# Optimization experiments

Hardware: AMD Instinct MI355X
Metric: run time of the kernel (lower is better)

Reference implementation:

```python
import jax, jax.numpy as jnp
import numpy as np

N_NODES = 100000
N_EDGES = 1600000
NUM_GRAPHS = 128
IN_DIM, HID, NCLS = 128, 64, 10


def setup_inputs() -> dict:
    key = jax.random.key(0)
    ks = jax.random.split(key, 12)
    inp = {
        'x': jax.random.normal(ks[0], (N_NODES, IN_DIM), jnp.float32),
        'edge_index': jax.random.randint(ks[1], (2, N_EDGES), 0, N_NODES),
        'edge_weight': jax.random.uniform(ks[2], (N_EDGES,), jnp.float32),
        'batch': jnp.sort(jax.random.randint(ks[3], (N_NODES,), 0, NUM_GRAPHS)),
        'W1': jax.random.normal(ks[4], (IN_DIM, HID), jnp.float32) * 0.05,
        'b1': jnp.zeros((HID,), jnp.float32),
        'W2': jax.random.normal(ks[5], (HID, HID), jnp.float32) * 0.05,
        'b2': jnp.zeros((HID,), jnp.float32),
        'Wc1': jax.random.normal(ks[6], (HID, HID // 2), jnp.float32) * 0.05,
        'bc1': jnp.zeros((HID // 2,), jnp.float32),
        'Wc2': jax.random.normal(ks[7], (HID // 2, NCLS), jnp.float32) * 0.05,
        'bc2': jnp.zeros((NCLS,), jnp.float32),
    }
    return inp


def _gcn_conv(x, row, col, ew, W, b, n):
    # PyG GCNConv: add self-loops (weight 1), symmetric normalization,
    # transform then aggregate: out[col] += norm * (xW)[row]
    loop = jnp.arange(n)
    r = jnp.concatenate([row, loop])
    c = jnp.concatenate([col, loop])
    w = jnp.concatenate([ew, jnp.ones((n,), ew.dtype)])
    deg = jax.ops.segment_sum(w, c, num_segments=n)
    dinv = jnp.where(deg > 0, jax.lax.rsqrt(deg), 0.0)
    norm = dinv[r] * w * dinv[c]          # [E+N]
    h = x @ W                              # [N, out]
    msg = h[r] * norm[:, None]             # [E+N, out]
    out = jax.ops.segment_sum(msg, c, num_segments=n)
    return out + b


def reference(x, edge_index, edge_weight, batch, W1, b1, W2, b2, Wc1, bc1, Wc2, bc2):
    n = x.shape[0]
    row, col = edge_index[0], edge_index[1]
    h = jax.nn.relu(_gcn_conv(x, row, col, edge_weight, W1, b1, n))
    # dropout p=0.5 is identity in eval mode
    h = jax.nn.relu(_gcn_conv(h, row, col, edge_weight, W2, b2, n))
    # global mean pool over batch indices
    sums = jax.ops.segment_sum(h, batch, num_segments=NUM_GRAPHS)
    cnts = jax.ops.segment_sum(jnp.ones((n,), h.dtype), batch, num_segments=NUM_GRAPHS)
    pooled = sums / jnp.clip(cnts, 1.0)[:, None]   # [G, HID]
    z = jax.nn.relu(pooled @ Wc1 + bc1)
    return z @ Wc2 + bc2                            # [G, NCLS]
```

## Files before the change

kernel.cpp:

```cpp
#include <hip/hip_runtime.h>
#include <hip/hip_fp16.h>


#define TPB 256
#define FIX_SCALE 16777216.0f
#define BKT_BITS 8
#define PART_BLOCKS 256

typedef _Float16 f16x8 __attribute__((ext_vector_type(8)));
typedef float f32x4 __attribute__((ext_vector_type(4)));

__device__ __forceinline__ int lower_bound_i(const int* __restrict__ a, int n, int key) {
    int lo = 0, hi = n;
    while (lo < hi) {
        int mid = (lo + hi) >> 1;
        if (a[mid] < key) lo = mid + 1; else hi = mid;
    }
    return lo;
}

__global__ __launch_bounds__(256) void k_histA(const int* __restrict__ col, int E, int CH,
                                               int K, int* __restrict__ bh) {
    __shared__ int hist[512];
    int b = blockIdx.x, t = threadIdx.x;
    for (int i = t; i < K; i += 256) hist[i] = 0;
    __syncthreads();
    int s = b * CH, e = min(E, s + CH);
    for (int i = s + t; i < e; i += 256) atomicAdd(&hist[col[i] >> BKT_BITS], 1);
    __syncthreads();
    for (int i = t; i < K; i += 256) bh[i * PART_BLOCKS + b] = hist[i];
}

__global__ void k_scan_partial(const int* __restrict__ cnt, int* __restrict__ bsums, int n) {
    __shared__ int red[4];
    int b = blockIdx.x, t = threadIdx.x;
    int base = b * 1024;
    int s = 0;
#pragma unroll
    for (int i = 0; i < 4; i++) {
        int idx = base + t + i * TPB;
        if (idx < n) s += cnt[idx];
    }
#pragma unroll
    for (int off = 32; off > 0; off >>= 1) s += __shfl_down(s, off);
    if ((t & 63) == 0) red[t >> 6] = s;
    __syncthreads();
    if (t == 0) bsums[b] = red[0] + red[1] + red[2] + red[3];
}

__global__ void k_scan_bsums(int* __restrict__ bsums, int nb) {
    int l = threadIdx.x;
    int carry = 0;
    for (int base = 0; base < nb; base += 64) {
        int i = base + l;
        int v = (i < nb) ? bsums[i] : 0;
        int orig = v;
#pragma unroll
        for (int off = 1; off < 64; off <<= 1) {
            int x = __shfl_up(v, off);
            if (l >= off) v += x;
        }
        if (i < nb) bsums[i] = v - orig + carry;
        carry += __shfl(v, 63);
    }
}

__global__ void k_scan_final(const int* __restrict__ cnt, const int* __restrict__ boffs,
                             int* __restrict__ offs, int n) {
    __shared__ int ts[TPB];
    int b = blockIdx.x, t = threadIdx.x;
    int base = b * 1024 + 4 * t;
    int v[4]; int s = 0;
#pragma unroll
    for (int i = 0; i < 4; i++) {
        int idx = base + i;
        v[i] = (idx < n) ? cnt[idx] : 0;
        s += v[i];
    }
    ts[t] = s; __syncthreads();
    for (int off = 1; off < 256; off <<= 1) {
        int x = (t >= off) ? ts[t - off] : 0;
        __syncthreads();
        ts[t] += x;
        __syncthreads();
    }
    int run = ts[t] - s + boffs[b];
#pragma unroll
    for (int i = 0; i < 4; i++) {
        int idx = base + i;
        if (idx < n) offs[idx] = run;
        run += v[i];
    }
}

__global__ __launch_bounds__(256) void k_partB(const int* __restrict__ row,
                                               const int* __restrict__ col,
                                               const float* __restrict__ ew,
                                               const int* __restrict__ bhs,
                                               int E, int CH, int K,
                                               int2* __restrict__ part2) {
    __shared__ int cur[512];
    int b = blockIdx.x, t = threadIdx.x;
    for (int i = t; i < K; i += 256) cur[i] = bhs[i * PART_BLOCKS + b];
    __syncthreads();
    int s = b * CH, e = min(E, s + CH);
    for (int i = s + t; i < e; i += 256) {
        int c = col[i];
        int pos = atomicAdd(&cur[c >> BKT_BITS], 1);
        part2[pos] = make_int2(row[i] | ((c & 255) << 20), __float_as_int(ew[i]));
    }
}

__global__ __launch_bounds__(256) void k_csrC(const int2* __restrict__ part2,
                                              const int* __restrict__ bhs,
                                              int K, int N, int E,
                                              int* __restrict__ offs, int* __restrict__ cnt,
                                              float* __restrict__ dinv,
                                              int2* __restrict__ csr) {
    __shared__ int lcnt[256];
    __shared__ unsigned lew[256];
    __shared__ int lcur[256];
    __shared__ int ts[256];
    int k = blockIdx.x, t = threadIdx.x;
    int n0 = k << BKT_BITS;
    lcnt[t] = 0; lew[t] = 0;
    __syncthreads();
    int estart = bhs[k * PART_BLOCKS];
    int eend   = (k + 1 < K) ? bhs[(k + 1) * PART_BLOCKS] : E;
    for (int i = estart + t; i < eend; i += 256) {
        int2 v = part2[i];
        int c = (v.x >> 20) & 255;
        atomicAdd(&lcnt[c], 1);
        float w = __int_as_float(v.y);
        atomicAdd(&lew[c], (unsigned)(w * FIX_SCALE + 0.5f));
    }
    __syncthreads();
    int myc = lcnt[t];
    ts[t] = myc; __syncthreads();
    for (int off = 1; off < 256; off <<= 1) {
        int x = (t >= off) ? ts[t - off] : 0;
        __syncthreads();
        ts[t] += x;
        __syncthreads();
    }
    int goff = estart + ts[t] - myc;
    int node = n0 + t;
    if (node < N) {
        offs[node] = goff;
        cnt[node]  = myc;
        float deg = 1.0f + (float)((double)lew[t] * (1.0 / 16777216.0));
        dinv[node] = 1.0f / sqrtf(deg);
    }
    lcur[t] = goff;
    __syncthreads();
    for (int i = estart + t; i < eend; i += 256) {
        int2 v = part2[i];
        int c = (v.x >> 20) & 255;
        int pos = atomicAdd(&lcur[c], 1);
        csr[pos] = make_int2(v.x & 0xFFFFF, v.y);
    }
}

__global__ void k_prepW(const float* __restrict__ W1, const float* __restrict__ W2,
                        __half* __restrict__ Wt1, __half* __restrict__ Wt2) {
    int t = threadIdx.x;
    for (int i = t; i < 64 * 128; i += 256) {
        int c = i >> 7, k = i & 127;
        Wt1[i] = (__half)W1[k * 64 + c];
    }
    for (int i = t; i < 64 * 64; i += 256) {
        int c = i >> 6, k = i & 63;
        Wt2[i] = (__half)W2[k * 64 + c];
    }
}

template <int K>
__global__ __launch_bounds__(256) void k_matmul_mfma(const float* __restrict__ X,
                                                     const __half* __restrict__ Wt,
                                                     const float* __restrict__ dinv,
                                                     __half* __restrict__ Hh, int n) {
    const int l = threadIdx.x & 63;
    const int w = threadIdx.x >> 6;
    const int rowBase = blockIdx.x * 64 + w * 16;
    const int r = l & 15;
    const int q = l >> 4;
    const int arow = rowBase + r;
    const bool rv = arow < n;

    f32x4 acc[4] = {{0.f, 0.f, 0.f, 0.f}, {0.f, 0.f, 0.f, 0.f},
                    {0.f, 0.f, 0.f, 0.f}, {0.f, 0.f, 0.f, 0.f}};

#pragma unroll
    for (int k0 = 0; k0 < K; k0 += 32) {
        f16x8 a = {};
        if (rv) {
            const float4 x0 = *reinterpret_cast<const float4*>(&X[(size_t)arow * K + k0 + 8 * q]);
            const float4 x1 = *reinterpret_cast<const float4*>(&X[(size_t)arow * K + k0 + 8 * q + 4]);
            a[0] = (_Float16)x0.x; a[1] = (_Float16)x0.y;
            a[2] = (_Float16)x0.z; a[3] = (_Float16)x0.w;
            a[4] = (_Float16)x1.x; a[5] = (_Float16)x1.y;
            a[6] = (_Float16)x1.z; a[7] = (_Float16)x1.w;
        }
#pragma unroll
        for (int ct = 0; ct < 4; ct++) {
            const f16x8 b = *reinterpret_cast<const f16x8*>(
                &Wt[(size_t)(ct * 16 + r) * K + k0 + 8 * q]);
            acc[ct] = __builtin_amdgcn_mfma_f32_16x16x32_f16(a, b, acc[ct], 0, 0, 0);
        }
    }

#pragma unroll
    for (int i = 0; i < 4; i++) {
        int r2 = rowBase + 4 * q + i;
        if (r2 < n) {
            float dv = dinv[r2];
#pragma unroll
            for (int ct = 0; ct < 4; ct++)
                Hh[(size_t)r2 * 64 + ct * 16 + r] = (__half)(acc[ct][i] * dv);
        }
    }
}

__global__ __launch_bounds__(256) void k_aggregate(
    const __half2* __restrict__ hp2, const int* __restrict__ offs,
    const int* __restrict__ cnt, const int2* __restrict__ csr,
    const float* __restrict__ dinv, const float* __restrict__ bias,
    float* __restrict__ out, int n) {
    const int lane = threadIdx.x & 63;
    const int epar = lane >> 5;
    const int lpos = lane & 31;
    const int node = blockIdx.x * 4 + (threadIdx.x >> 6);
    if (node >= n) return;
    const int c = cnt[node];
    const int s = offs[node];

    int2 mc = make_int2(node, 0);
    if (lane < c) mc = csr[s + lane];
    const int cc = min(c, 64);
    const int npairs = (cc + 1) >> 1;
    const int p8 = (npairs + 7) & ~7;

    float ax[8] = {0.f, 0.f, 0.f, 0.f, 0.f, 0.f, 0.f, 0.f};
    float ay[8] = {0.f, 0.f, 0.f, 0.f, 0.f, 0.f, 0.f, 0.f};

    for (int p = 0; p < p8; p += 8) {
#pragma unroll
        for (int i = 0; i < 8; i++) {
            int idx = 2 * (p + i) + epar;
            int src = __shfl(mc.x, idx);
            float w = __int_as_float(__shfl(mc.y, idx));
            float2 f = __half22float2(hp2[(size_t)src * 32 + lpos]);
            ax[i] = fmaf(f.x, w, ax[i]);
            ay[i] = fmaf(f.y, w, ay[i]);
        }
    }
    float tx = ((ax[0] + ax[1]) + (ax[2] + ax[3])) + ((ax[4] + ax[5]) + (ax[6] + ax[7]));
    float ty = ((ay[0] + ay[1]) + (ay[2] + ay[3])) + ((ay[4] + ay[5]) + (ay[6] + ay[7]));
    tx += __shfl(tx, lane ^ 32);
    ty += __shfl(ty, lane ^ 32);

    for (int j = 64; j < c; ++j) {
        int2 e = csr[s + j];
        float2 f = __half22float2(hp2[(size_t)e.x * 32 + lpos]);
        float w = __int_as_float(e.y);
        tx = fmaf(f.x, w, tx);
        ty = fmaf(f.y, w, ty);
    }

    if (epar == 0) {
        float2 sv = __half22float2(hp2[(size_t)node * 32 + lpos]);
        const float2 bv = *reinterpret_cast<const float2*>(&bias[lpos * 2]);
        float dv = dinv[node];
        float rx = fmaf(tx + sv.x, dv, bv.x);
        float ry = fmaf(ty + sv.y, dv, bv.y);
        float2 o = make_float2(fmaxf(rx, 0.f), fmaxf(ry, 0.f));
        *reinterpret_cast<float2*>(&out[(size_t)node * 64 + lpos * 2]) = o;
    }
}

__global__ __launch_bounds__(1024) void k_pool_head(
    const float* __restrict__ h, const int* __restrict__ batch, int n,
    const float* __restrict__ Wc1, const float* __restrict__ bc1,
    const float* __restrict__ Wc2, const float* __restrict__ bc2,
    float* __restrict__ out) {
    const int g = blockIdx.x;
    const int t = threadIdx.x;
    const int lane = t & 63, w = t >> 6;
    __shared__ float sums[16][64];
    __shared__ float pooled[64];
    __shared__ float z[32];

    int start = lower_bound_i(batch, n, g);
    int end   = lower_bound_i(batch, n, g + 1);

    float acc = 0.f;
    for (int i = start + w; i < end; i += 16)
        acc += h[(size_t)i * 64 + lane];
    sums[w][lane] = acc;
    __syncthreads();
    if (w == 0) {
        float v = 0.f;
#pragma unroll
        for (int k = 0; k < 16; k++) v += sums[k][lane];
        float c = (float)(end - start);
        pooled[lane] = v / fmaxf(c, 1.0f);
    }
    __syncthreads();
    if (t < 32) {
        float a = bc1[t];
        for (int k = 0; k < 64; k++) a = fmaf(pooled[k], Wc1[k * 32 + t], a);
        z[t] = fmaxf(a, 0.f);
    }
    __syncthreads();
    if (t < 10) {
        float a = bc2[t];
        for (int k = 0; k < 32; k++) a = fmaf(z[k], Wc2[k * 10 + t], a);
        out[g * 10 + t] = a;
    }
}

extern "C" void kernel_launch(void* const* d_in, const int* in_sizes, int n_in,
                              void* d_out, int out_size, void* d_ws, size_t ws_size,
                              hipStream_t stream) {
    const float* x    = (const float*)d_in[0];
    const int*   ei   = (const int*)d_in[1];
    const float* ew   = (const float*)d_in[2];
    const int*   bat  = (const int*)d_in[3];
    const float* W1   = (const float*)d_in[4];
    const float* b1   = (const float*)d_in[5];
    const float* W2   = (const float*)d_in[6];
    const float* b2   = (const float*)d_in[7];
    const float* Wc1  = (const float*)d_in[8];
    const float* bc1  = (const float*)d_in[9];
    const float* Wc2  = (const float*)d_in[10];
    const float* bc2  = (const float*)d_in[11];
    float* out = (float*)d_out;

    const int N = in_sizes[0] / 128;
    const int E = in_sizes[2];
    const int G = out_size / 10;
    const int K = (N + 255) >> BKT_BITS;
    const int KB = K * PART_BLOCKS;
    const int CH = (E + PART_BLOCKS - 1) / PART_BLOCKS;

    const int* row = ei;
    const int* col = ei + E;

    char* p = (char*)d_ws;
    auto alloc = [&](size_t bytes) -> void* {
        void* r = (void*)p;
        p += (bytes + 255) & ~(size_t)255;
        return r;
    };
    int*    bh    = (int*)   alloc((size_t)KB * 4);
    int*    bhs   = (int*)   alloc((size_t)KB * 4);
    int*    bsums = (int*)   alloc(8192);
    int*    offs  = (int*)   alloc((size_t)N * 4);
    int*    cnt   = (int*)   alloc((size_t)N * 4);
    float*  dinv  = (float*) alloc((size_t)N * 4);
    __half* Wt1   = (__half*)alloc(64 * 128 * 2);
    __half* Wt2   = (__half*)alloc(64 * 64 * 2);
    int2*   csr   = (int2*)  alloc((size_t)E * 8);
    size_t hbytes = (size_t)N * 64 * 2;
    size_t pbytes = (size_t)E * 8;
    char*   hbase = (char*)  alloc(hbytes > pbytes ? hbytes : pbytes);
    float*  o     = (float*) alloc((size_t)N * 64 * 4);
    int2*   part2 = (int2*)  hbase;
    __half* h     = (__half*)hbase;

    const int NB = (KB + 1023) / 1024;

    k_prepW<<<1, 256, 0, stream>>>(W1, W2, Wt1, Wt2);

    k_histA<<<PART_BLOCKS, 256, 0, stream>>>(col, E, CH, K, bh);
    k_scan_partial<<<NB, TPB, 0, stream>>>(bh, bsums, KB);
    k_scan_bsums<<<1, 64, 0, stream>>>(bsums, NB);
    k_scan_final<<<NB, TPB, 0, stream>>>(bh, bsums, bhs, KB);
    k_partB<<<PART_BLOCKS, 256, 0, stream>>>(row, col, ew, bhs, E, CH, K, part2);
    k_csrC<<<K, 256, 0, stream>>>(part2, bhs, K, N, E, offs, cnt, dinv, csr);

    const int gb_mm = (N + 63) / 64;
    const int gb_ag = (N + 3) / 4;

    k_matmul_mfma<128><<<gb_mm, 256, 0, stream>>>(x, Wt1, dinv, h, N);
    k_aggregate<<<gb_ag, 256, 0, stream>>>((const __half2*)h, offs, cnt, csr, dinv, b1, o, N);
    k_matmul_mfma<64><<<gb_mm, 256, 0, stream>>>(o, Wt2, dinv, h, N);
    k_aggregate<<<gb_ag, 256, 0, stream>>>((const __half2*)h, offs, cnt, csr, dinv, b2, o, N);
    k_pool_head<<<G, 1024, 0, stream>>>(o, bat, N, Wc1, bc1, Wc2, bc2, out);
}
```

Baseline: 198.7 us.

## Store aggregate outputs in fp16, split pooling across blocks, fold weight prep

The aggregate kernels now write their hidden activations as fp16 instead of fp32. The second matmul reads those fp16 values directly, and the pooling stage reads them too, which halves the intermediate traffic. Pooling is split into 4 slices per graph (512 blocks) plus a small head kernel, replacing 128 blocks of 1024 threads, to spread the reduction over more CUs. The weight transpose kernel is folded into block 0 of the histogram kernel, saving one launch. Storing the activations in fp16 adds some rounding error, and the new pooling path adds an extra launch and a partial-sum buffer.

```diff
diff --git a/kernel.cpp b/kernel.cpp
--- a/kernel.cpp
+++ b/kernel.cpp
@@ -20,9 +20,23 @@
 }
 
 __global__ __launch_bounds__(256) void k_histA(const int* __restrict__ col, int E, int CH,
-                                               int K, int* __restrict__ bh) {
+                                               int K, int* __restrict__ bh,
+                                               const float* __restrict__ W1,
+                                               const float* __restrict__ W2,
+                                               __half* __restrict__ Wt1,
+                                               __half* __restrict__ Wt2) {
     __shared__ int hist[512];
     int b = blockIdx.x, t = threadIdx.x;
+    if (b == 0) {
+        for (int i = t; i < 64 * 128; i += 256) {
+            int c = i >> 7, k = i & 127;
+            Wt1[i] = (__half)W1[k * 64 + c];
+        }
+        for (int i = t; i < 64 * 64; i += 256) {
+            int c = i >> 6, k = i & 63;
+            Wt2[i] = (__half)W2[k * 64 + c];
+        }
+    }
     for (int i = t; i < K; i += 256) hist[i] = 0;
     __syncthreads();
     int s = b * CH, e = min(E, s + CH);
@@ -161,21 +175,8 @@
     }
 }
 
-__global__ void k_prepW(const float* __restrict__ W1, const float* __restrict__ W2,
-                        __half* __restrict__ Wt1, __half* __restrict__ Wt2) {
-    int t = threadIdx.x;
-    for (int i = t; i < 64 * 128; i += 256) {
-        int c = i >> 7, k = i & 127;
-        Wt1[i] = (__half)W1[k * 64 + c];
-    }
-    for (int i = t; i < 64 * 64; i += 256) {
-        int c = i >> 6, k = i & 63;
-        Wt2[i] = (__half)W2[k * 64 + c];
-    }
-}
-
-template <int K>
-__global__ __launch_bounds__(256) void k_matmul_mfma(const float* __restrict__ X,
+template <int K, bool FP32IN>
+__global__ __launch_bounds__(256) void k_matmul_mfma(const void* __restrict__ Xv,
                                                      const __half* __restrict__ Wt,
                                                      const float* __restrict__ dinv,
                                                      __half* __restrict__ Hh, int n) {
@@ -194,12 +195,18 @@
     for (int k0 = 0; k0 < K; k0 += 32) {
         f16x8 a = {};
         if (rv) {
-            const float4 x0 = *reinterpret_cast<const float4*>(&X[(size_t)arow * K + k0 + 8 * q]);
-            const float4 x1 = *reinterpret_cast<const float4*>(&X[(size_t)arow * K + k0 + 8 * q + 4]);
-            a[0] = (_Float16)x0.x; a[1] = (_Float16)x0.y;
-            a[2] = (_Float16)x0.z; a[3] = (_Float16)x0.w;
-            a[4] = (_Float16)x1.x; a[5] = (_Float16)x1.y;
-            a[6] = (_Float16)x1.z; a[7] = (_Float16)x1.w;
+            if constexpr (FP32IN) {
+                const float* X = (const float*)Xv;
+                const float4 x0 = *reinterpret_cast<const float4*>(&X[(size_t)arow * K + k0 + 8 * q]);
+                const float4 x1 = *reinterpret_cast<const float4*>(&X[(size_t)arow * K + k0 + 8 * q + 4]);
+                a[0] = (_Float16)x0.x; a[1] = (_Float16)x0.y;
+                a[2] = (_Float16)x0.z; a[3] = (_Float16)x0.w;
+                a[4] = (_Float16)x1.x; a[5] = (_Float16)x1.y;
+                a[6] = (_Float16)x1.z; a[7] = (_Float16)x1.w;
+            } else {
+                const _Float16* X = (const _Float16*)Xv;
+                a = *reinterpret_cast<const f16x8*>(&X[(size_t)arow * K + k0 + 8 * q]);
+            }
         }
 #pragma unroll
         for (int ct = 0; ct < 4; ct++) {
@@ -225,7 +232,7 @@
     const __half2* __restrict__ hp2, const int* __restrict__ offs,
     const int* __restrict__ cnt, const int2* __restrict__ csr,
     const float* __restrict__ dinv, const float* __restrict__ bias,
-    float* __restrict__ out, int n) {
+    __half2* __restrict__ outh, int n) {
     const int lane = threadIdx.x & 63;
     const int epar = lane >> 5;
     const int lpos = lane & 31;
@@ -271,49 +278,66 @@
         float2 sv = __half22float2(hp2[(size_t)node * 32 + lpos]);
         const float2 bv = *reinterpret_cast<const float2*>(&bias[lpos * 2]);
         float dv = dinv[node];
-        float rx = fmaf(tx + sv.x, dv, bv.x);
-        float ry = fmaf(ty + sv.y, dv, bv.y);
-        float2 o = make_float2(fmaxf(rx, 0.f), fmaxf(ry, 0.f));
-        *reinterpret_cast<float2*>(&out[(size_t)node * 64 + lpos * 2]) = o;
-    }
-}
-
-__global__ __launch_bounds__(1024) void k_pool_head(
-    const float* __restrict__ h, const int* __restrict__ batch, int n,
+        float rx = fmaxf(fmaf(tx + sv.x, dv, bv.x), 0.f);
+        float ry = fmaxf(fmaf(ty + sv.y, dv, bv.y), 0.f);
+        outh[(size_t)node * 32 + lpos] = __floats2half2_rn(rx, ry);
+    }
+}
+
+__global__ __launch_bounds__(256) void k_pool4(
+    const __half* __restrict__ oh, const int* __restrict__ batch, int n,
+    float* __restrict__ psum) {
+    const int g = blockIdx.x >> 2;
+    const int sl = blockIdx.x & 3;
+    const int t = threadIdx.x;
+    const int lane = t & 63, w = t >> 6;
+    __shared__ float sums[4][64];
+
+    int start = lower_bound_i(batch, n, g);
+    int end   = lower_bound_i(batch, n, g + 1);
+    int len   = end - start;
+    int s0 = start + (len * sl) / 4;
+    int s1 = start + (len * (sl + 1)) / 4;
+
+    float acc = 0.f;
+    for (int i = s0 + w; i < s1; i += 4)
+        acc += __half2float(oh[(size_t)i * 64 + lane]);
+    sums[w][lane] = acc;
+    __syncthreads();
+    if (w == 0) {
+        float v = sums[0][lane] + sums[1][lane] + sums[2][lane] + sums[3][lane];
+        psum[(size_t)blockIdx.x * 64 + lane] = v;
+    }
+}
+
+__global__ __launch_bounds__(64) void k_head(
+    const float* __restrict__ psum, const int* __restrict__ batch, int n,
     const float* __restrict__ Wc1, const float* __restrict__ bc1,
     const float* __restrict__ Wc2, const float* __restrict__ bc2,
     float* __restrict__ out) {
     const int g = blockIdx.x;
     const int t = threadIdx.x;
-    const int lane = t & 63, w = t >> 6;
-    __shared__ float sums[16][64];
     __shared__ float pooled[64];
     __shared__ float z[32];
 
     int start = lower_bound_i(batch, n, g);
     int end   = lower_bound_i(batch, n, g + 1);
-
-    float acc = 0.f;
-    for (int i = start + w; i < end; i += 16)
-        acc += h[(size_t)i * 64 + lane];
-    sums[w][lane] = acc;
-    __syncthreads();
-    if (w == 0) {
-        float v = 0.f;
-#pragma unroll
-        for (int k = 0; k < 16; k++) v += sums[k][lane];
-        float c = (float)(end - start);
-        pooled[lane] = v / fmaxf(c, 1.0f);
-    }
+    float ccount = (float)(end - start);
+
+    float v = psum[(size_t)(g * 4 + 0) * 64 + t] + psum[(size_t)(g * 4 + 1) * 64 + t] +
+              psum[(size_t)(g * 4 + 2) * 64 + t] + psum[(size_t)(g * 4 + 3) * 64 + t];
+    pooled[t] = v / fmaxf(ccount, 1.0f);
     __syncthreads();
     if (t < 32) {
         float a = bc1[t];
+#pragma unroll
         for (int k = 0; k < 64; k++) a = fmaf(pooled[k], Wc1[k * 32 + t], a);
         z[t] = fmaxf(a, 0.f);
     }
     __syncthreads();
     if (t < 10) {
         float a = bc2[t];
+#pragma unroll
         for (int k = 0; k < 32; k++) a = fmaf(z[k], Wc2[k * 10 + t], a);
         out[g * 10 + t] = a;
     }
@@ -360,19 +384,18 @@
     float*  dinv  = (float*) alloc((size_t)N * 4);
     __half* Wt1   = (__half*)alloc(64 * 128 * 2);
     __half* Wt2   = (__half*)alloc(64 * 64 * 2);
+    float*  psum  = (float*) alloc((size_t)G * 4 * 64 * 4);
     int2*   csr   = (int2*)  alloc((size_t)E * 8);
     size_t hbytes = (size_t)N * 64 * 2;
     size_t pbytes = (size_t)E * 8;
     char*   hbase = (char*)  alloc(hbytes > pbytes ? hbytes : pbytes);
-    float*  o     = (float*) alloc((size_t)N * 64 * 4);
+    __half* o     = (__half*)alloc((size_t)N * 64 * 2);
     int2*   part2 = (int2*)  hbase;
     __half* h     = (__half*)hbase;
 
     const int NB = (KB + 1023) / 1024;
 
-    k_prepW<<<1, 256, 0, stream>>>(W1, W2, Wt1, Wt2);
-
-    k_histA<<<PART_BLOCKS, 256, 0, stream>>>(col, E, CH, K, bh);
+    k_histA<<<PART_BLOCKS, 256, 0, stream>>>(col, E, CH, K, bh, W1, W2, Wt1, Wt2);
     k_scan_partial<<<NB, TPB, 0, stream>>>(bh, bsums, KB);
     k_scan_bsums<<<1, 64, 0, stream>>>(bsums, NB);
     k_scan_final<<<NB, TPB, 0, stream>>>(bh, bsums, bhs, KB);
@@ -382,9 +405,12 @@
     const int gb_mm = (N + 63) / 64;
     const int gb_ag = (N + 3) / 4;
 
-    k_matmul_mfma<128><<<gb_mm, 256, 0, stream>>>(x, Wt1, dinv, h, N);
-    k_aggregate<<<gb_ag, 256, 0, stream>>>((const __half2*)h, offs, cnt, csr, dinv, b1, o, N);
-    k_matmul_mfma<64><<<gb_mm, 256, 0, stream>>>(o, Wt2, dinv, h, N);
-    k_aggregate<<<gb_ag, 256, 0, stream>>>((const __half2*)h, offs, cnt, csr, dinv, b2, o, N);
-    k_pool_head<<<G, 1024, 0, stream>>>(o, bat, N, Wc1, bc1, Wc2, bc2, out);
-}
+    k_matmul_mfma<128, true><<<gb_mm, 256, 0, stream>>>(x, Wt1, dinv, h, N);
+    k_aggregate<<<gb_ag, 256, 0, stream>>>((const __half2*)h, offs, cnt, csr, dinv, b1,
+                                           (__half2*)o, N);
+    k_matmul_mfma<64, false><<<gb_mm, 256, 0, stream>>>(o, Wt2, dinv, h, N);
+    k_aggregate<<<gb_ag, 256, 0, stream>>>((const __half2*)h, offs, cnt, csr, dinv, b2,
+                                           (__half2*)o, N);
+    k_pool4<<<G * 4, 256, 0, stream>>>(o, bat, N, psum);
+    k_head<<<G, 64, 0, stream>>>(psum, bat, N, Wc1, bc1, Wc2, bc2, out);
+}
```

Result: no change. 199.9 us (+0.6%).
